# Performance work log

Measured on AMD Instinct MI355X. Metric: run time of the kernel, lower is better.

Reference implementation:

```python
import jax, jax.numpy as jnp
import numpy as np

THETA = 10000.0
NUM_HEADS = 16


def apply_rope(x, pos, theta):
    # x: [..., s, d_k] with d_k even; pos: [s] (broadcasts over leading dims)
    d_k = x.shape[-1]
    inv_freq = 1.0 / (theta ** (jnp.arange(0, d_k, 2, dtype=x.dtype) / d_k))  # [d_k/2]
    ang = pos.astype(x.dtype)[..., None] * inv_freq  # [s, d_k/2]
    cos, sin = jnp.cos(ang), jnp.sin(ang)
    xr = x.reshape(x.shape[:-1] + (d_k // 2, 2))
    x0, x1 = xr[..., 0], xr[..., 1]
    out0 = x0 * cos - x1 * sin
    out1 = x0 * sin + x1 * cos
    return jnp.stack((out0, out1), axis=-1).reshape(x.shape)


def setup_inputs() -> dict:
    key = jax.random.key(0)
    ks = jax.random.split(key, 5)
    B, S, D = 4, 2048, 1024
    sigma = 2.0 / (D + D) ** 0.5
    return {
        "x": jax.random.normal(ks[0], (B, S, D), dtype=jnp.float32),
        "token_positions": jnp.arange(S, dtype=jnp.int64 if jax.config.jax_enable_x64 else jnp.int32),
        "wq": jax.random.normal(ks[1], (D, D), dtype=jnp.float32) * sigma,
        "wk": jax.random.normal(ks[2], (D, D), dtype=jnp.float32) * sigma,
        "wv": jax.random.normal(ks[3], (D, D), dtype=jnp.float32) * sigma,
        "wo": jax.random.normal(ks[4], (D, D), dtype=jnp.float32) * sigma,
    }


def reference(x, token_positions, wq, wk, wv, wo):
    B, S, D = x.shape
    H = NUM_HEADS
    d_k = D // H

    def proj(w, t):  # weight [out, in], t [..., in]
        return jnp.einsum('oi,bsi->bso', w, t)

    def heads(t):  # [b, s, (h d)] -> [b, h, s, d]
        return t.reshape(B, S, H, d_k).transpose(0, 2, 1, 3)

    Q = heads(proj(wq, x))
    K = heads(proj(wk, x))
    V = heads(proj(wv, x))
    Q = apply_rope(Q, token_positions, THETA)
    K = apply_rope(K, token_positions, THETA)

    scores = jnp.einsum('bhqd,bhkd->bhqk', Q, K) * (d_k ** -0.5)
    causal = jnp.tril(jnp.ones((S, S), dtype=bool))
    scores = jnp.where(causal, scores, -jnp.inf)
    attn = jax.nn.softmax(scores.astype(jnp.float32), axis=-1).astype(scores.dtype)
    out = jnp.einsum('bhqk,bhkd->bhqd', attn, V)
    out = out.transpose(0, 2, 1, 3).reshape(B, S, D)
    return jnp.einsum('oi,bsi->bso', wo, out)
```

## Files before the change

kernel.cpp:

```cpp
#include <hip/hip_runtime.h>
#include <cstdint>
#include <cstddef>

#define Bv 4
#define Sv 2048
#define Hv 16
#define Dv 1024
#define Mv (Bv*Sv)

typedef __attribute__((ext_vector_type(8))) short short8;
typedef __attribute__((ext_vector_type(8))) unsigned short ushort8v;
typedef __attribute__((ext_vector_type(4))) float f32x4;

__device__ inline float bf2f(unsigned short u) {
  union { unsigned int i; float f; } x; x.i = ((unsigned int)u) << 16; return x.f;
}
__device__ inline unsigned short f2bf(float f) {
  union { float f; unsigned int i; } x; x.f = f;
  unsigned int r = x.i + 0x7FFFu + ((x.i >> 16) & 1u);
  return (unsigned short)(r >> 16);
}

typedef __attribute__((address_space(1))) const unsigned short gu16;
typedef __attribute__((address_space(3))) unsigned short lu16;
__device__ inline void gld_lds16(const unsigned short* g, unsigned short* l) {
  __builtin_amdgcn_global_load_lds((gu16*)g, (lu16*)l, 16, 0, 0);
}

__global__ __launch_bounds__(256) void prep_all(
    const float* __restrict__ x, const float* __restrict__ wq,
    const float* __restrict__ wk, const float* __restrict__ wv,
    const float* __restrict__ wo, const int* __restrict__ pos,
    unsigned short* __restrict__ xb, unsigned short* __restrict__ wqkvb,
    unsigned short* __restrict__ wob, float* __restrict__ tab) {
  const int bb = blockIdx.x, tid = threadIdx.x;
  if (bb < 8192) {
    int i = bb * 256 + tid;
    float4 v = reinterpret_cast<const float4*>(x)[i];
    ushort4 o;
    o.x = f2bf(v.x); o.y = f2bf(v.y); o.z = f2bf(v.z); o.w = f2bf(v.w);
    reinterpret_cast<ushort4*>(xb)[i] = o;
  } else if (bb < 11264) {
    int i = (bb - 8192) * 256 + tid;
    int w = i >> 18, off = i & 262143;
    const float* src = (w == 0) ? wq : (w == 1) ? wk : wv;
    float4 v = reinterpret_cast<const float4*>(src)[off];
    ushort4 o;
    o.x = f2bf(v.x); o.y = f2bf(v.y); o.z = f2bf(v.z); o.w = f2bf(v.w);
    reinterpret_cast<ushort4*>(wqkvb)[i] = o;
  } else if (bb < 12288) {
    int i = (bb - 11264) * 256 + tid;
    float4 v = reinterpret_cast<const float4*>(wo)[i];
    ushort4 o;
    o.x = f2bf(v.x); o.y = f2bf(v.y); o.z = f2bf(v.z); o.w = f2bf(v.w);
    reinterpret_cast<ushort4*>(wob)[i] = o;
  } else {
    int idx = (bb - 12288) * 256 + tid;
    int s = idx >> 5, i = idx & 31;
    float p = (float)pos[s];
    float a = p * __builtin_exp2f(-0.41524101186092027f * (float)i);
    tab[(s << 6) + i]      = __builtin_cosf(a);
    tab[(s << 6) + 32 + i] = __builtin_sinf(a);
  }
}

__device__ __forceinline__ void xcd_swizzle(int& bm, int& bn) {
  const int nx = gridDim.x;
  const int nwg = nx * gridDim.y;
  int flat = blockIdx.y * nx + blockIdx.x;
  if ((nwg & 7) == 0) {
    int q = nwg >> 3;
    flat = (flat & 7) * q + (flat >> 3);
  }
  bm = (flat / nx) * 128;
  bn = (flat % nx) * 128;
}

__device__ inline void storeC(float* p, float v) { *p = v; }
__device__ inline void storeC(unsigned short* p, float v) { *p = f2bf(v); }

template <typename CT>
__global__ __launch_bounds__(256) void gemm_bt_128(
    const unsigned short* __restrict__ A,
    const unsigned short* __restrict__ B,
    CT* __restrict__ C,
    int M, int N, int K) {
  __shared__ unsigned short As[128 * 64];
  __shared__ unsigned short Bs[128 * 64];
  const int tid = threadIdx.x;
  const int wave = tid >> 6, lane = tid & 63;
  int bm, bn;
  xcd_swizzle(bm, bn);
  const int wr = (wave >> 1) * 64, wc = (wave & 1) * 64;

  f32x4 acc[4][4] = {};

  int srow[4], scol[4];
#pragma unroll
  for (int i = 0; i < 4; ++i) {
    int c = i * 4 + wave;
    srow[i] = c * 8 + (lane >> 3);
    scol[i] = ((lane & 7) ^ ((lane >> 3) & 7)) * 8;
  }

  const int fr = lane & 15;
  const int g_ = lane >> 4;
  int offA[2][4], offB[2][4];
#pragma unroll
  for (int kh = 0; kh < 2; ++kh)
#pragma unroll
    for (int m = 0; m < 4; ++m) {
      offA[kh][m] = (wr + m * 16 + fr) * 64 + ((((kh << 2) + g_) ^ (fr & 7)) * 8);
      offB[kh][m] = (wc + m * 16 + fr) * 64 + ((((kh << 2) + g_) ^ (fr & 7)) * 8);
    }

  const int nt = K >> 6;
  auto STAGE = [&](int t) {
    const int k0 = t << 6;
#pragma unroll
    for (int i = 0; i < 4; ++i) {
      gld_lds16(A + (size_t)(bm + srow[i]) * K + k0 + scol[i], &As[(i * 4 + wave) * 512]);
      gld_lds16(B + (size_t)(bn + srow[i]) * K + k0 + scol[i], &Bs[(i * 4 + wave) * 512]);
    }
  };

  STAGE(0);
  __syncthreads();

  for (int t = 0; t < nt; ++t) {
    short8 af[4], bfr[4];
#pragma unroll
    for (int m = 0; m < 4; m++)
      af[m] = *reinterpret_cast<const short8*>(&As[offA[0][m]]);
#pragma unroll
    for (int n = 0; n < 4; n++)
      bfr[n] = *reinterpret_cast<const short8*>(&Bs[offB[0][n]]);
#pragma unroll
    for (int m = 0; m < 4; m++)
#pragma unroll
      for (int n = 0; n < 4; n++)
        acc[m][n] = __builtin_amdgcn_mfma_f32_16x16x32_bf16(af[m], bfr[n], acc[m][n], 0, 0, 0);
    short8 af1[4], bf1[4];
#pragma unroll
    for (int m = 0; m < 4; m++)
      af1[m] = *reinterpret_cast<const short8*>(&As[offA[1][m]]);
#pragma unroll
    for (int n = 0; n < 4; n++)
      bf1[n] = *reinterpret_cast<const short8*>(&Bs[offB[1][n]]);
    __syncthreads();
    if (t + 1 < nt) STAGE(t + 1);
#pragma unroll
    for (int m = 0; m < 4; m++)
#pragma unroll
      for (int n = 0; n < 4; n++)
        acc[m][n] = __builtin_amdgcn_mfma_f32_16x16x32_bf16(af1[m], bf1[n], acc[m][n], 0, 0, 0);
    __syncthreads();
  }

  const int er = (lane >> 4) * 4, ec = lane & 15;
#pragma unroll
  for (int m = 0; m < 4; m++)
#pragma unroll
    for (int n = 0; n < 4; n++)
#pragma unroll
      for (int r = 0; r < 4; r++) {
        int row = bm + wr + m * 16 + er + r;
        int col = bn + wc + n * 16 + ec;
        storeC(&C[(size_t)row * N + col], acc[m][n][r]);
      }
}

__global__ __launch_bounds__(256) void gemm_qkv(
    const unsigned short* __restrict__ A,
    const unsigned short* __restrict__ B,
    unsigned short* __restrict__ Qp,
    unsigned short* __restrict__ Kp,
    unsigned short* __restrict__ Vt,
    const float* __restrict__ tab) {
  const int K = Dv;
  __shared__ unsigned short As[128 * 64];
  __shared__ unsigned short Bs[128 * 64];
  const int tid = threadIdx.x;
  const int wave = tid >> 6, lane = tid & 63;
  int bm, bn;
  xcd_swizzle(bm, bn);
  const int wr = (wave >> 1) * 64, wc = (wave & 1) * 64;

  f32x4 acc[4][4] = {};

  int srow[4], scol[4];
#pragma unroll
  for (int i = 0; i < 4; ++i) {
    int c = i * 4 + wave;
    srow[i] = c * 8 + (lane >> 3);
    scol[i] = ((lane & 7) ^ ((lane >> 3) & 7)) * 8;
  }

  const int fr = lane & 15;
  const int g_ = lane >> 4;
  int offA[2][4], offB[2][4];
#pragma unroll
  for (int kh = 0; kh < 2; ++kh)
#pragma unroll
    for (int m = 0; m < 4; ++m) {
      offA[kh][m] = (wr + m * 16 + fr) * 64 + ((((kh << 2) + g_) ^ (fr & 7)) * 8);
      offB[kh][m] = (wc + m * 16 + fr) * 64 + ((((kh << 2) + g_) ^ (fr & 7)) * 8);
    }

  const int nt = K >> 6;
  auto STAGE = [&](int t) {
    const int k0 = t << 6;
#pragma unroll
    for (int i = 0; i < 4; ++i) {
      gld_lds16(A + (size_t)(bm + srow[i]) * K + k0 + scol[i], &As[(i * 4 + wave) * 512]);
      gld_lds16(B + (size_t)(bn + srow[i]) * K + k0 + scol[i], &Bs[(i * 4 + wave) * 512]);
    }
  };

  STAGE(0);
  __syncthreads();

  for (int t = 0; t < nt; ++t) {
    short8 af[4], bfr[4];
#pragma unroll
    for (int m = 0; m < 4; m++)
      af[m] = *reinterpret_cast<const short8*>(&As[offA[0][m]]);
#pragma unroll
    for (int n = 0; n < 4; n++)
      bfr[n] = *reinterpret_cast<const short8*>(&Bs[offB[0][n]]);
#pragma unroll
    for (int m = 0; m < 4; m++)
#pragma unroll
      for (int n = 0; n < 4; n++)
        acc[m][n] = __builtin_amdgcn_mfma_f32_16x16x32_bf16(af[m], bfr[n], acc[m][n], 0, 0, 0);
    short8 af1[4], bf1[4];
#pragma unroll
    for (int m = 0; m < 4; m++)
      af1[m] = *reinterpret_cast<const short8*>(&As[offA[1][m]]);
#pragma unroll
    for (int n = 0; n < 4; n++)
      bf1[n] = *reinterpret_cast<const short8*>(&Bs[offB[1][n]]);
    __syncthreads();
    if (t + 1 < nt) STAGE(t + 1);
#pragma unroll
    for (int m = 0; m < 4; m++)
#pragma unroll
      for (int n = 0; n < 4; n++)
        acc[m][n] = __builtin_amdgcn_mfma_f32_16x16x32_bf16(af1[m], bf1[n], acc[m][n], 0, 0, 0);
    __syncthreads();
  }

  const int er = (lane >> 4) * 4, ec = lane & 15;
  const int region = bn >> 10;
  if (region < 2) {
    unsigned short* T = (region == 0) ? Qp : Kp;
#pragma unroll
    for (int m = 0; m < 4; m++)
#pragma unroll
      for (int n = 0; n < 4; n++) {
        const int col = bn + wc + n * 16 + ec;
        const int ccol = col & (Dv - 1);
        const int ii = (ccol & 63) >> 1;
        const bool odd = col & 1;
#pragma unroll
        for (int r = 0; r < 4; r++) {
          int row = bm + wr + m * 16 + er + r;
          int s = row & (Sv - 1);
          float v = acc[m][n][r];
          float pv = __shfl_xor(v, 1);
          float cc = tab[(s << 6) + ii];
          float sn = tab[(s << 6) + 32 + ii];
          float o = odd ? __builtin_fmaf(pv, sn, v * cc)
                        : __builtin_fmaf(v, cc, -(pv * sn));
          T[(size_t)row * Dv + ccol] = f2bf(o);
        }
      }
  } else {
#pragma unroll
    for (int m = 0; m < 4; m++)
#pragma unroll
      for (int n = 0; n < 4; n++) {
        const int dfull = (bn - 2048) + wc + n * 16 + ec;
        const int row0 = bm + wr + m * 16 + er;
        const int bb = row0 >> 11, s = row0 & (Sv - 1);
        const size_t vtrow = ((size_t)bb * 16 + (dfull >> 6)) * 64 + (dfull & 63);
        ushort4 ov;
        ov.x = f2bf(acc[m][n][0]);
        ov.y = f2bf(acc[m][n][1]);
        ov.z = f2bf(acc[m][n][2]);
        ov.w = f2bf(acc[m][n][3]);
        *reinterpret_cast<ushort4*>(Vt + vtrow * Sv + s) = ov;
      }
  }
}

template <bool MASKED>
__device__ __forceinline__ void softmax_strip(
    f32x4 (&sacc)[2][4], const int qrel0,
    float (&mrun2)[2], float (&lrun)[2], f32x4 (&oacc)[2][4],
    unsigned int (&pk)[2][4][2]) {
  const float c1 = 0.18033688011112042f;
#pragma unroll
  for (int qf = 0; qf < 2; ++qf) {
    const int qrel = qrel0 + qf * 16;
    float pv[4][4];
    float mx = -INFINITY;
#pragma unroll
    for (int kf = 0; kf < 4; ++kf)
#pragma unroll
      for (int r = 0; r < 4; ++r) {
        float s = sacc[qf][kf][r];
        if (MASKED) s = (kf * 16 + r > qrel) ? -INFINITY : s;
        pv[kf][r] = s;
        mx = fmaxf(mx, s);
      }
    mx = fmaxf(mx, __shfl_xor(mx, 16));
    mx = fmaxf(mx, __shfl_xor(mx, 32));
    float pm = mx * c1;
    if (__any(pm > mrun2[qf] + 8.0f)) {
      float m2 = fmaxf(mrun2[qf], pm);
      float sfq = __builtin_exp2f(mrun2[qf] - m2);
      lrun[qf] *= sfq;
#pragma unroll
      for (int dc = 0; dc < 4; ++dc)
#pragma unroll
        for (int r = 0; r < 4; ++r) oacc[qf][dc][r] *= sfq;
      mrun2[qf] = m2;
    }
    const float nm = -mrun2[qf];
    float ps = 0.f;
#pragma unroll
    for (int kf = 0; kf < 4; ++kf)
#pragma unroll
      for (int r = 0; r < 4; ++r) {
        float p = __builtin_exp2f(__builtin_fmaf(pv[kf][r], c1, nm));
        ps += p;
        pv[kf][r] = p;
      }
    ps += __shfl_xor(ps, 16);
    ps += __shfl_xor(ps, 32);
    lrun[qf] += ps;
#pragma unroll
    for (int kf = 0; kf < 4; ++kf)
#pragma unroll
      for (int hh = 0; hh < 2; ++hh) {
        unsigned int rr;
        asm("v_cvt_pk_bf16_f32 %0, %1, %2"
            : "=v"(rr) : "v"(pv[kf][2 * hh]), "v"(pv[kf][2 * hh + 1]));
        pk[qf][kf][hh] = rr;
      }
  }
}

__device__ __forceinline__ void pv_strip(
    const short8 (&vfr)[2][4], const unsigned int (&pk)[2][4][2],
    f32x4 (&oacc)[2][4], const int idx0, const int idx1, const bool hi) {
#pragma unroll
  for (int ks = 0; ks < 2; ++ks)
#pragma unroll
    for (int qf = 0; qf < 2; ++qf) {
      int ra = __builtin_amdgcn_ds_bpermute(idx0, (int)pk[qf][2 * ks][0]);
      int rb = __builtin_amdgcn_ds_bpermute(idx0, (int)pk[qf][2 * ks + 1][0]);
      int rc = __builtin_amdgcn_ds_bpermute(idx0, (int)pk[qf][2 * ks][1]);
      int rd = __builtin_amdgcn_ds_bpermute(idx0, (int)pk[qf][2 * ks + 1][1]);
      int re = __builtin_amdgcn_ds_bpermute(idx1, (int)pk[qf][2 * ks][0]);
      int rf = __builtin_amdgcn_ds_bpermute(idx1, (int)pk[qf][2 * ks + 1][0]);
      int rg = __builtin_amdgcn_ds_bpermute(idx1, (int)pk[qf][2 * ks][1]);
      int rh = __builtin_amdgcn_ds_bpermute(idx1, (int)pk[qf][2 * ks + 1][1]);
      union { unsigned int u[4]; short8 v; } pw;
      pw.u[0] = hi ? (unsigned)rb : (unsigned)ra;
      pw.u[1] = hi ? (unsigned)rd : (unsigned)rc;
      pw.u[2] = hi ? (unsigned)rf : (unsigned)re;
      pw.u[3] = hi ? (unsigned)rh : (unsigned)rg;
      __builtin_amdgcn_s_setprio(1);
#pragma unroll
      for (int dc = 0; dc < 4; ++dc)
        oacc[qf][dc] = __builtin_amdgcn_mfma_f32_16x16x32_bf16(vfr[ks][dc], pw.v, oacc[qf][dc], 0, 0, 0);
      __builtin_amdgcn_s_setprio(0);
    }
}

__global__ __launch_bounds__(256, 2) void attn_mfma(
    const unsigned short* __restrict__ Q,
    const unsigned short* __restrict__ K,
    const unsigned short* __restrict__ Vt,
    unsigned short* __restrict__ O) {
  __shared__ __align__(16) unsigned short ldsK[3][4096];
  __shared__ __align__(16) unsigned short ldsV[3][4096];
  const int tid = threadIdx.x;
  const int wave = tid >> 6, lane = tid & 63;
  const int g = lane >> 4, m = lane & 15;
  const int F = blockIdx.x;
  const int q7 = F >> 3;
  const int bh = ((F & 7) << 3) | (q7 & 7);
  const int bi = q7 >> 3;
  const int b = bh >> 4, h = bh & 15;
  const int j = bi * 4 + wave;
  const int sA = j, sB = 63 - j;
  const int qA0 = sA * 32, qB0 = sB * 32;
  const int ntA = (sA >> 1) + 1, ntB = (sB >> 1) + 1;
  const int ntBmax = ((63 - bi * 4) >> 1) + 1;
  const size_t qkbase = ((size_t)b * Sv) * Dv + (size_t)h * 64;
  const size_t vtbase = (size_t)bh * 64 * Sv;
  const f32x4 zf = {0.f, 0.f, 0.f, 0.f};

  int srowS[2], scolS[2];
#pragma unroll
  for (int i = 0; i < 2; ++i) {
    int s = ((i * 4 + wave) << 6) + lane;
    int s2 = s ^ ((s >> 3) & 7);
    srowS[i] = s2 >> 3;
    scolS[i] = (s2 & 7) * 8;
  }

  short8 qA[2][2], qB[2][2];
#pragma unroll
  for (int qf = 0; qf < 2; ++qf)
#pragma unroll
    for (int ks = 0; ks < 2; ++ks) {
      qA[qf][ks] = *reinterpret_cast<const short8*>(
          Q + qkbase + (size_t)(qA0 + qf * 16 + m) * Dv + ks * 32 + g * 8);
      qB[qf][ks] = *reinterpret_cast<const short8*>(
          Q + qkbase + (size_t)(qB0 + qf * 16 + m) * Dv + ks * 32 + g * 8);
    }

  int offL[2][4];
#pragma unroll
  for (int ks = 0; ks < 2; ++ks)
#pragma unroll
    for (int f = 0; f < 4; ++f)
      offL[ks][f] = (f * 16 + m) * 64 + ((((ks << 2) + g) ^ (m & 7)) * 8);

  f32x4 oA[2][4] = {}, oB[2][4] = {};
  float mA[2] = {-INFINITY, -INFINITY}, mB[2] = {-INFINITY, -INFINITY};
  float lA[2] = {0.f, 0.f}, lB[2] = {0.f, 0.f};

  const int idx0 = (((g & 1) << 5) + m) << 2;
  const int idx1 = idx0 + 64;
  const bool hi = (g >= 2);
  int qrelA = qA0 + m - 4 * g;
  int qrelB = qB0 + m - 4 * g;

  auto STAGE = [&](int c, int t) {
    const int kb = t << 6;
#pragma unroll
    for (int i = 0; i < 2; ++i) {
      gld_lds16(K + qkbase + (size_t)(kb + srowS[i]) * Dv + scolS[i],
                &ldsK[c][(i * 4 + wave) * 512]);
      gld_lds16(Vt + vtbase + (size_t)srowS[i] * Sv + kb + scolS[i],
                &ldsV[c][(i * 4 + wave) * 512]);
    }
  };

  STAGE(0, 0);
  STAGE(1, 1);
  int cur = 0, bs = 2;

  for (int t = 0; t < ntBmax; ++t) {
    if (t + 1 < ntBmax) {
      asm volatile("s_waitcnt vmcnt(4)" ::: "memory");
    } else {
      asm volatile("s_waitcnt vmcnt(0)" ::: "memory");
    }
    __builtin_amdgcn_sched_barrier(0);
    __builtin_amdgcn_s_barrier();
    if (t + 2 < ntBmax) STAGE(bs, t + 2);

    if (t < ntB) {
      const bool actA = (t < ntA);
      f32x4 sAacc[2][4], sBacc[2][4];
      short8 kfr[4];
#pragma unroll
      for (int kf = 0; kf < 4; ++kf)
        kfr[kf] = *reinterpret_cast<const short8*>(&ldsK[cur][offL[0][kf]]);
      __builtin_amdgcn_s_setprio(1);
#pragma unroll
      for (int qf = 0; qf < 2; ++qf)
#pragma unroll
        for (int kf = 0; kf < 4; ++kf)
          sBacc[qf][kf] = __builtin_amdgcn_mfma_f32_16x16x32_bf16(kfr[kf], qB[qf][0], zf, 0, 0, 0);
      if (actA)
#pragma unroll
        for (int qf = 0; qf < 2; ++qf)
#pragma unroll
          for (int kf = 0; kf < 4; ++kf)
            sAacc[qf][kf] = __builtin_amdgcn_mfma_f32_16x16x32_bf16(kfr[kf], qA[qf][0], zf, 0, 0, 0);
      __builtin_amdgcn_s_setprio(0);
#pragma unroll
      for (int kf = 0; kf < 4; ++kf)
        kfr[kf] = *reinterpret_cast<const short8*>(&ldsK[cur][offL[1][kf]]);
      __builtin_amdgcn_s_setprio(1);
#pragma unroll
      for (int qf = 0; qf < 2; ++qf)
#pragma unroll
        for (int kf = 0; kf < 4; ++kf)
          sBacc[qf][kf] = __builtin_amdgcn_mfma_f32_16x16x32_bf16(kfr[kf], qB[qf][1], sBacc[qf][kf], 0, 0, 0);
      if (actA)
#pragma unroll
        for (int qf = 0; qf < 2; ++qf)
#pragma unroll
          for (int kf = 0; kf < 4; ++kf)
            sAacc[qf][kf] = __builtin_amdgcn_mfma_f32_16x16x32_bf16(kfr[kf], qA[qf][1], sAacc[qf][kf], 0, 0, 0);
      __builtin_amdgcn_s_setprio(0);

      short8 vfr[2][4];
#pragma unroll
      for (int ks = 0; ks < 2; ++ks)
#pragma unroll
        for (int dc = 0; dc < 4; ++dc)
          vfr[ks][dc] = *reinterpret_cast<const short8*>(&ldsV[cur][offL[ks][dc]]);

      unsigned int pkB[2][4][2], pkA[2][4][2];
      if (t == ntB - 1) softmax_strip<true >(sBacc, qrelB, mB, lB, oB, pkB);
      else              softmax_strip<false>(sBacc, qrelB, mB, lB, oB, pkB);
      if (actA) {
        if (t == ntA - 1) softmax_strip<true >(sAacc, qrelA, mA, lA, oA, pkA);
        else              softmax_strip<false>(sAacc, qrelA, mA, lA, oA, pkA);
      }
      pv_strip(vfr, pkB, oB, idx0, idx1, hi);
      if (actA) pv_strip(vfr, pkA, oA, idx0, idx1, hi);

      qrelA -= 64; qrelB -= 64;
    }

    cur = (cur == 2) ? 0 : cur + 1;
    bs = (bs == 2) ? 0 : bs + 1;
  }

#pragma unroll
  for (int qf = 0; qf < 2; ++qf) {
    float rnA = 1.0f / lA[qf];
    float rnB = 1.0f / lB[qf];
    size_t rowA = (size_t)(qA0 + qf * 16 + m);
    size_t rowB = (size_t)(qB0 + qf * 16 + m);
#pragma unroll
    for (int dc = 0; dc < 4; ++dc) {
      ushort4 ov;
      ov.x = f2bf(oA[qf][dc][0] * rnA);
      ov.y = f2bf(oA[qf][dc][1] * rnA);
      ov.z = f2bf(oA[qf][dc][2] * rnA);
      ov.w = f2bf(oA[qf][dc][3] * rnA);
      *reinterpret_cast<ushort4*>(O + qkbase + rowA * Dv + dc * 16 + 4 * g) = ov;
      ov.x = f2bf(oB[qf][dc][0] * rnB);
      ov.y = f2bf(oB[qf][dc][1] * rnB);
      ov.z = f2bf(oB[qf][dc][2] * rnB);
      ov.w = f2bf(oB[qf][dc][3] * rnB);
      *reinterpret_cast<ushort4*>(O + qkbase + rowB * Dv + dc * 16 + 4 * g) = ov;
    }
  }
}

extern "C" void kernel_launch(void* const* d_in, const int* in_sizes, int n_in,
                              void* d_out, int out_size, void* d_ws, size_t ws_size,
                              hipStream_t stream) {
  const float* x   = (const float*)d_in[0];
  const int*   pos = (const int*)d_in[1];
  const float* wq  = (const float*)d_in[2];
  const float* wk  = (const float*)d_in[3];
  const float* wv  = (const float*)d_in[4];
  const float* wo  = (const float*)d_in[5];
  float* out = (float*)d_out;

  char* w = (char*)d_ws;
  unsigned short* xb    = (unsigned short*)(w);
  unsigned short* wqkvb = (unsigned short*)(w + (16u << 20));
  unsigned short* wob   = (unsigned short*)(w + (22u << 20));
  unsigned short* Qp    = (unsigned short*)(w + (24u << 20));
  unsigned short* Kp    = (unsigned short*)(w + (40u << 20));
  unsigned short* Vt    = (unsigned short*)(w + (56u << 20));
  float*          tab   = (float*)(w + (72u << 20));

  prep_all<<<12544, 256, 0, stream>>>(x, wq, wk, wv, wo, pos, xb, wqkvb, wob, tab);

  gemm_qkv<<<dim3(3 * Dv / 128, Mv / 128), 256, 0, stream>>>(xb, wqkvb, Qp, Kp, Vt, tab);

  attn_mfma<<<512, 256, 0, stream>>>(Qp, Kp, Vt, xb);

  gemm_bt_128<float><<<dim3(Dv / 128, Mv / 128), 256, 0, stream>>>(xb, wob, out, Mv, Dv, Dv);
}
```

Measured before the change: 200.6 us.

## Rewrite QKV GEMM with 256x256 tiles, 8 waves, double-buffered LDS pipeline

The QKV projection GEMM now uses 256x256 output tiles with 512 threads (8 waves, each computing 128x64), in place of 128x128 tiles with 4 waves. It double-buffers LDS and splits the next tile's loads into four quarter stages interleaved with the MFMA phases, using s_setprio and raw barriers. Block indices are remapped with a custom XCD swizzle for the 384-block grid. The larger tiles are meant to improve operand reuse and overlap global loads with compute, at the cost of 128 KB of LDS and higher register pressure, which limits occupancy and leaves fewer blocks than CUs.

```diff
diff --git a/kernel.cpp b/kernel.cpp
--- a/kernel.cpp
+++ b/kernel.cpp
@@ -170,84 +170,91 @@
       }
 }
 
-__global__ __launch_bounds__(256) void gemm_qkv(
+__global__ __launch_bounds__(512, 2) void gemm_qkv_256(
     const unsigned short* __restrict__ A,
-    const unsigned short* __restrict__ B,
+    const unsigned short* __restrict__ Bw,
     unsigned short* __restrict__ Qp,
     unsigned short* __restrict__ Kp,
     unsigned short* __restrict__ Vt,
     const float* __restrict__ tab) {
   const int K = Dv;
-  __shared__ unsigned short As[128 * 64];
-  __shared__ unsigned short Bs[128 * 64];
+  __shared__ unsigned short As[2][16384];
+  __shared__ unsigned short Bs[2][16384];
   const int tid = threadIdx.x;
   const int wave = tid >> 6, lane = tid & 63;
-  int bm, bn;
-  xcd_swizzle(bm, bn);
-  const int wr = (wave >> 1) * 64, wc = (wave & 1) * 64;
-
-  f32x4 acc[4][4] = {};
-
-  int srow[4], scol[4];
-#pragma unroll
-  for (int i = 0; i < 4; ++i) {
-    int c = i * 4 + wave;
-    srow[i] = c * 8 + (lane >> 3);
-    scol[i] = ((lane & 7) ^ ((lane >> 3) & 7)) * 8;
-  }
+  const int wm = wave >> 2, wn = wave & 3;
+  int flat = blockIdx.x;
+  flat = (flat & 7) * 48 + (flat >> 3);
+  const int bm = (flat / 12) * 256;
+  const int bn = (flat % 12) * 256;
+  const int wr = wm * 128, wc = wn * 64;
+
+  f32x4 acc[8][4] = {};
+
+  const int scolS = ((lane & 7) ^ (lane >> 3)) * 8;
+  int srowS[2];
+#pragma unroll
+  for (int i = 0; i < 2; ++i) srowS[i] = (i * 8 + wave) * 8 + (lane >> 3);
 
   const int fr = lane & 15;
   const int g_ = lane >> 4;
-  int offA[2][4], offB[2][4];
-#pragma unroll
-  for (int kh = 0; kh < 2; ++kh)
-#pragma unroll
-    for (int m = 0; m < 4; ++m) {
-      offA[kh][m] = (wr + m * 16 + fr) * 64 + ((((kh << 2) + g_) ^ (fr & 7)) * 8);
-      offB[kh][m] = (wc + m * 16 + fr) * 64 + ((((kh << 2) + g_) ^ (fr & 7)) * 8);
-    }
-
-  const int nt = K >> 6;
-  auto STAGE = [&](int t) {
+  int colp[2];
+#pragma unroll
+  for (int kk = 0; kk < 2; ++kk) colp[kk] = (((kk << 2) + g_) ^ (fr & 7)) * 8;
+  int rowA[8], rowB[4];
+#pragma unroll
+  for (int mi = 0; mi < 8; ++mi) rowA[mi] = (wr + mi * 16 + fr) * 64;
+#pragma unroll
+  for (int n = 0; n < 4; ++n) rowB[n] = (wc + n * 16 + fr) * 64;
+
+  auto STAGE_HALF = [&](int h, int t, int b) {
     const int k0 = t << 6;
-#pragma unroll
-    for (int i = 0; i < 4; ++i) {
-      gld_lds16(A + (size_t)(bm + srow[i]) * K + k0 + scol[i], &As[(i * 4 + wave) * 512]);
-      gld_lds16(B + (size_t)(bn + srow[i]) * K + k0 + scol[i], &Bs[(i * 4 + wave) * 512]);
-    }
+    const unsigned short* src;
+    unsigned short* dst;
+    int rowbase;
+    if (h < 2) { src = A;  rowbase = bm + h * 128;       dst = &As[b][h * 8192]; }
+    else       { src = Bw; rowbase = bn + (h - 2) * 128; dst = &Bs[b][(h - 2) * 8192]; }
+#pragma unroll
+    for (int i = 0; i < 2; ++i)
+      gld_lds16(src + (size_t)(rowbase + srowS[i]) * K + k0 + scolS,
+                dst + (i * 8 + wave) * 512);
   };
 
-  STAGE(0);
+  const int nkt = K >> 6;
+#pragma unroll
+  for (int h = 0; h < 4; ++h) STAGE_HALF(h, 0, 0);
   __syncthreads();
-
-  for (int t = 0; t < nt; ++t) {
-    short8 af[4], bfr[4];
-#pragma unroll
-    for (int m = 0; m < 4; m++)
-      af[m] = *reinterpret_cast<const short8*>(&As[offA[0][m]]);
-#pragma unroll
-    for (int n = 0; n < 4; n++)
-      bfr[n] = *reinterpret_cast<const short8*>(&Bs[offB[0][n]]);
-#pragma unroll
-    for (int m = 0; m < 4; m++)
-#pragma unroll
-      for (int n = 0; n < 4; n++)
-        acc[m][n] = __builtin_amdgcn_mfma_f32_16x16x32_bf16(af[m], bfr[n], acc[m][n], 0, 0, 0);
-    short8 af1[4], bf1[4];
-#pragma unroll
-    for (int m = 0; m < 4; m++)
-      af1[m] = *reinterpret_cast<const short8*>(&As[offA[1][m]]);
-#pragma unroll
-    for (int n = 0; n < 4; n++)
-      bf1[n] = *reinterpret_cast<const short8*>(&Bs[offB[1][n]]);
-    __syncthreads();
-    if (t + 1 < nt) STAGE(t + 1);
-#pragma unroll
-    for (int m = 0; m < 4; m++)
-#pragma unroll
-      for (int n = 0; n < 4; n++)
-        acc[m][n] = __builtin_amdgcn_mfma_f32_16x16x32_bf16(af1[m], bf1[n], acc[m][n], 0, 0, 0);
-    __syncthreads();
+  int cur = 0;
+
+  for (int t = 0; t < nkt; ++t) {
+    const bool more = (t + 1 < nkt);
+#pragma unroll
+    for (int p = 0; p < 4; ++p) {
+      const int mh = p >> 1, kk = p & 1;
+      short8 af[4], bf[4];
+#pragma unroll
+      for (int j = 0; j < 4; ++j)
+        af[j] = *reinterpret_cast<const short8*>(&As[cur][rowA[mh * 4 + j] + colp[kk]]);
+#pragma unroll
+      for (int n = 0; n < 4; ++n)
+        bf[n] = *reinterpret_cast<const short8*>(&Bs[cur][rowB[n] + colp[kk]]);
+      if (more) STAGE_HALF(p, t + 1, cur ^ 1);
+      __builtin_amdgcn_s_barrier();
+      __builtin_amdgcn_s_setprio(1);
+#pragma unroll
+      for (int j = 0; j < 4; ++j)
+#pragma unroll
+        for (int n = 0; n < 4; ++n)
+          acc[mh * 4 + j][n] =
+              __builtin_amdgcn_mfma_f32_16x16x32_bf16(af[j], bf[n], acc[mh * 4 + j][n], 0, 0, 0);
+      __builtin_amdgcn_s_setprio(0);
+      if (p == 3 && more) {
+        asm volatile("s_waitcnt vmcnt(0)" ::: "memory");
+        __builtin_amdgcn_sched_barrier(0);
+      }
+      __builtin_amdgcn_s_barrier();
+    }
+    cur ^= 1;
   }
 
   const int er = (lane >> 4) * 4, ec = lane & 15;
@@ -255,7 +262,7 @@
   if (region < 2) {
     unsigned short* T = (region == 0) ? Qp : Kp;
 #pragma unroll
-    for (int m = 0; m < 4; m++)
+    for (int mi = 0; mi < 8; mi++)
 #pragma unroll
       for (int n = 0; n < 4; n++) {
         const int col = bn + wc + n * 16 + ec;
@@ -264,9 +271,9 @@
         const bool odd = col & 1;
 #pragma unroll
         for (int r = 0; r < 4; r++) {
-          int row = bm + wr + m * 16 + er + r;
+          int row = bm + wr + mi * 16 + er + r;
           int s = row & (Sv - 1);
-          float v = acc[m][n][r];
+          float v = acc[mi][n][r];
           float pv = __shfl_xor(v, 1);
           float cc = tab[(s << 6) + ii];
           float sn = tab[(s << 6) + 32 + ii];
@@ -277,18 +284,18 @@
       }
   } else {
 #pragma unroll
-    for (int m = 0; m < 4; m++)
+    for (int mi = 0; mi < 8; mi++)
 #pragma unroll
       for (int n = 0; n < 4; n++) {
         const int dfull = (bn - 2048) + wc + n * 16 + ec;
-        const int row0 = bm + wr + m * 16 + er;
+        const int row0 = bm + wr + mi * 16 + er;
         const int bb = row0 >> 11, s = row0 & (Sv - 1);
         const size_t vtrow = ((size_t)bb * 16 + (dfull >> 6)) * 64 + (dfull & 63);
         ushort4 ov;
-        ov.x = f2bf(acc[m][n][0]);
-        ov.y = f2bf(acc[m][n][1]);
-        ov.z = f2bf(acc[m][n][2]);
-        ov.w = f2bf(acc[m][n][3]);
+        ov.x = f2bf(acc[mi][n][0]);
+        ov.y = f2bf(acc[mi][n][1]);
+        ov.z = f2bf(acc[mi][n][2]);
+        ov.w = f2bf(acc[mi][n][3]);
         *reinterpret_cast<ushort4*>(Vt + vtrow * Sv + s) = ov;
       }
   }
@@ -572,7 +579,7 @@
 
   prep_all<<<12544, 256, 0, stream>>>(x, wq, wk, wv, wo, pos, xb, wqkvb, wob, tab);
 
-  gemm_qkv<<<dim3(3 * Dv / 128, Mv / 128), 256, 0, stream>>>(xb, wqkvb, Qp, Kp, Vt, tab);
+  gemm_qkv_256<<<384, 512, 0, stream>>>(xb, wqkvb, Qp, Kp, Vt, tab);
 
   attn_mfma<<<512, 256, 0, stream>>>(Qp, Kp, Vt, xb);
 
```

Measured after the change: 219.1 us. +9.2%, slower.
